# Performance work log

Hardware: AMD Instinct MI355X
Metric: run time of the kernel (lower is better)

Reference implementation:

```python
import jax, jax.numpy as jnp
import numpy as np

H, N_FULL, L_KERNEL, CHANNELS, RANK = 256, 128, 2048, 1, 1


def _legs_nplr(N, rank=1):
    # HiPPO-LegS transition + rank-1 correction -> NPLR (diag w - P P^*) form.
    q = np.arange(N, dtype=np.float64)
    col, row = np.meshgrid(q, q)
    r = 2 * q + 1
    M = -(np.where(row >= col, r, 0) - np.diag(q))
    T = np.sqrt(np.diag(2 * q + 1))
    A = T @ M @ np.linalg.inv(T)
    B = np.diag(T)                        # (N,)
    P = np.sqrt(0.5 + q)[None, :]         # (rank=1, N)
    AP = A + (P[:, :, None] * P[:, None, :]).sum(0)
    w, V = np.linalg.eig(AP)              # complex eigendecomposition
    w = w[0::2]                           # keep one of each conjugate pair -> N//2
    V = V[:, 0::2]
    V_inv = V.conj().T
    Bc = V_inv @ B.astype(V.dtype)        # (N//2,)
    Pc = (V_inv @ P.T.astype(V.dtype)).T  # (rank, N//2)
    return w, Pc, Bc


def _c2r(a):
    return jnp.stack([jnp.real(a), jnp.imag(a)], axis=-1).astype(jnp.float32)


def _r2c(a):
    return jax.lax.complex(a[..., 0], a[..., 1])


def setup_inputs() -> dict:
    key = jax.random.key(0)
    k1, k2 = jax.random.split(key)
    w, P, B = _legs_nplr(N_FULL, RANK)    # numpy complex128, half-size N = 64
    Nh = w.shape[-1]
    w = jnp.asarray(np.broadcast_to(w[None, :], (H, Nh)).copy())
    P = jnp.asarray(np.broadcast_to(P[:, None, :], (RANK, H, Nh)).copy())
    B = jnp.asarray(np.broadcast_to(B[None, None, :], (1, H, Nh)).copy())
    C = jax.random.normal(k1, (CHANNELS, H, Nh, 2), dtype=jnp.float32)
    log_dt = jax.random.uniform(k2, (H,), dtype=jnp.float32) * (
        float(np.log(0.1)) - float(np.log(0.001))) + float(np.log(0.001))
    return {
        'w_ri': _c2r(w), 'P_ri': _c2r(P), 'B_ri': _c2r(B),
        'C_ri': C, 'log_dt': log_dt, 'L': L_KERNEL,
    }


def reference(w_ri, P_ri, B_ri, C_ri, log_dt, L):
    w = _r2c(w_ri)        # (H, N) complex64
    P = _r2c(P_ri)        # (r, H, N)
    B = _r2c(B_ri)        # (1, H, N)
    C = _r2c(C_ri)        # (c, H, N)
    dt = jnp.exp(log_dt)  # (H,)
    Lh = L // 2 + 1
    # FFT nodes, processed through the bilinear transform
    omega = jnp.exp((-2j * np.pi / L) * jnp.arange(Lh, dtype=jnp.float32))
    z = 2 * (1 - omega) / (1 + omega)
    w_dt = w * dt[:, None]                               # incorporate dt into A
    Bcat = jnp.concatenate([B, P], axis=0)               # (1+r, H, N)
    Ccat = jnp.concatenate([C, jnp.conj(P)], axis=0)     # (c+r, H, N)  Q = conj(P)
    v = Bcat[:, None] * Ccat[None]                       # (1+r, c+r, H, N)
    # conjugate-symmetric extension to the full 2N poles
    v2 = jnp.concatenate([v, jnp.conj(v)], axis=-1)      # (1+r, c+r, H, 2N)
    w2 = jnp.concatenate([w_dt, jnp.conj(w_dt)], axis=-1)  # (H, 2N)
    # naive Cauchy sum (the O(N*L) hotspot): (1+r, c+r, H, Lh)
    r = (v2[..., None] / (z - w2[..., None])).sum(axis=-2)
    r = r * dt[None, None, :, None]
    # rank-1 Woodbury correction for the low-rank term
    k_f = r[:-1, :-1] - r[:-1, -1:] * r[-1:, :-1] / (1 + r[-1:, -1:])
    # final bilinear-transform correction, then frequency -> time
    k_f = k_f * 2 / (1 + omega)
    k = jnp.fft.irfft(k_f, n=L, axis=-1)                 # (1, c, H, L) real
    return k[0].astype(jnp.float32)                      # (c, H, L)
```

## Files before the change

kernel.cpp:

```cpp
#include <hip/hip_runtime.h>

#define NH 64
#define LFULL 2048
#define MH 1024
#define PI_F 3.14159265358979323846f
#define ANG_HALF 1.5339807878856412e-3f

typedef __attribute__((ext_vector_type(2))) float f32x2;
typedef __attribute__((ext_vector_type(4))) float f32x4;

#define SV(v, i, j) __builtin_shufflevector((v), (v), (i), (j))
#define PK_FMA(acc, a_, b_) asm("v_pk_fma_f32 %0, %1, %2, %0" : "+v"(acc) : "v"(a_), "v"(b_))

struct QS2 { f32x2 s1, s2, s3, s4; };

__global__ __launch_bounds__(512) void hippo_ssk(
    const float* __restrict__ w_ri,
    const float* __restrict__ P_ri,
    const float* __restrict__ B_ri,
    const float* __restrict__ C_ri,
    const float* __restrict__ log_dt,
    float* __restrict__ out)
{
    __shared__ __attribute__((aligned(16))) float pole2[NH][20];
    __shared__ float2 Kf[MH + 1];
    __shared__ float2 bufA[MH];
    __shared__ float2 bufB[MH];

    const int h   = blockIdx.x;
    const int tid = threadIdx.x;

    if (tid < NH) {
        const float dt = __expf(log_dt[h]);
        const float2 w = ((const float2*)w_ri)[h*NH + tid];
        const float2 P = ((const float2*)P_ri)[h*NH + tid];
        const float2 B = ((const float2*)B_ri)[h*NH + tid];
        const float2 C = ((const float2*)C_ri)[h*NH + tid];
        const float a = w.x * dt, b = w.y * dt;
        const float v00r = (B.x*C.x - B.y*C.y) * dt;
        const float v00i = (B.x*C.y + B.y*C.x) * dt;
        const float v01r = (B.x*P.x + B.y*P.y) * dt;
        const float v01i = (B.y*P.x - B.x*P.y) * dt;
        const float v10r = (P.x*C.x - P.y*C.y) * dt;
        const float v10i = (P.x*C.y + P.y*C.x) * dt;
        const float v11  = (P.x*P.x + P.y*P.y) * dt;
        float* pp = pole2[tid];
        const float na2 = -2.f*a;
        const float m2  = fmaf(a, a, b*b);
        const float p1_00 = -2.f*fmaf(v00r, a, v00i*b), p0_00 = 2.f*v00r;
        const float p1_01 = -2.f*fmaf(v01r, a, v01i*b), p0_01 = 2.f*v01r;
        const float p1_10 = -2.f*fmaf(v10r, a, v10i*b), p0_10 = 2.f*v10r;
        const float p1_11 = -2.f*v11*a,                 p0_11 = 2.f*v11;
        pp[0]=na2;   pp[1]=na2;   pp[2]=m2;    pp[3]=m2;
        pp[4]=p1_00; pp[5]=p1_00; pp[6]=p0_00; pp[7]=p0_00;
        pp[8]=p1_01; pp[9]=p1_01; pp[10]=p0_01; pp[11]=p0_01;
        pp[12]=p1_10; pp[13]=p1_10; pp[14]=p0_10; pp[15]=p0_10;
        pp[16]=p1_11; pp[17]=p1_11; pp[18]=p0_11; pp[19]=p0_11;
        float s = v00r;
        #pragma unroll
        for (int off = 32; off > 0; off >>= 1) s += __shfl_down(s, off, 64);
        if (tid == 0) Kf[MH] = make_float2(s, 0.f);
    }
    __syncthreads();

    {
        const int lA = tid;
        const int lB = tid + 512;
        float shA, chA, shB, chB;
        __sincosf(ANG_HALF * (float)lA, &shA, &chA);
        __sincosf(ANG_HALF * (float)lB, &shB, &chB);
        const float yA = 2.f * shA * __builtin_amdgcn_rcpf(chA);
        const float yB = 2.f * shB * __builtin_amdgcn_rcpf(chB);
        f32x2 yp;  yp.x = yA;        yp.y = yB;
        f32x2 ny2; ny2.x = -yA*yA;   ny2.y = -yB*yB;
        QS2 a00 = {{0,0},{0,0},{0,0},{0,0}};
        QS2 a01 = {{0,0},{0,0},{0,0},{0,0}};
        QS2 a10 = {{0,0},{0,0},{0,0},{0,0}};
        QS2 a11 = {{0,0},{0,0},{0,0},{0,0}};
        #pragma unroll 4
        for (int n = 0; n < NH; ++n) {
            const f32x4 c0 = *reinterpret_cast<const f32x4*>(&pole2[n][0]);
            const f32x4 c1 = *reinterpret_cast<const f32x4*>(&pole2[n][4]);
            const f32x4 c2 = *reinterpret_cast<const f32x4*>(&pole2[n][8]);
            const f32x4 c3 = *reinterpret_cast<const f32x4*>(&pole2[n][12]);
            const f32x4 c4 = *reinterpret_cast<const f32x4*>(&pole2[n][16]);
            const f32x2 dr = SV(c0, 2, 3) + ny2;
            const f32x2 di = SV(c0, 0, 1) * yp;
            const f32x2 den = dr*dr + di*di;
            f32x2 t;
            t.x = __builtin_amdgcn_rcpf(den.x);
            t.y = __builtin_amdgcn_rcpf(den.y);
            const f32x2 U = dr * t;
            const f32x2 V = di * t;
            PK_FMA(a00.s1, SV(c1,0,1), U);  PK_FMA(a00.s2, SV(c1,0,1), V);
            PK_FMA(a00.s3, SV(c1,2,3), U);  PK_FMA(a00.s4, SV(c1,2,3), V);
            PK_FMA(a01.s1, SV(c2,0,1), U);  PK_FMA(a01.s2, SV(c2,0,1), V);
            PK_FMA(a01.s3, SV(c2,2,3), U);  PK_FMA(a01.s4, SV(c2,2,3), V);
            PK_FMA(a10.s1, SV(c3,0,1), U);  PK_FMA(a10.s2, SV(c3,0,1), V);
            PK_FMA(a10.s3, SV(c3,2,3), U);  PK_FMA(a10.s4, SV(c3,2,3), V);
            PK_FMA(a11.s1, SV(c4,0,1), U);  PK_FMA(a11.s2, SV(c4,0,1), V);
            PK_FMA(a11.s3, SV(c4,2,3), U);  PK_FMA(a11.s4, SV(c4,2,3), V);
        }
        const f32x2 r00r = yp*a00.s4 + a00.s1;
        const f32x2 r00i = yp*a00.s3 - a00.s2;
        const f32x2 r01r = yp*a01.s4 + a01.s1;
        const f32x2 r01i = yp*a01.s3 - a01.s2;
        const f32x2 r10r = yp*a10.s4 + a10.s1;
        const f32x2 r10i = yp*a10.s3 - a10.s2;
        const f32x2 r11r = yp*a11.s4 + a11.s1;
        const f32x2 r11i = yp*a11.s3 - a11.s2;
        const f32x2 nr = r01r*r10r - r01i*r10i;
        const f32x2 ni = r01r*r10i + r01i*r10r;
        const f32x2 dw = 1.f + r11r;
        const f32x2 dv = r11i;
        f32x2 id2;
        id2.x = 1.f / (dw.x*dw.x + dv.x*dv.x);
        id2.y = 1.f / (dw.y*dw.y + dv.y*dv.y);
        const f32x2 cr = (nr*dw + ni*dv)*id2;
        const f32x2 ci = (ni*dw - nr*dv)*id2;
        const f32x2 k0r = r00r - cr;
        const f32x2 k0i = r00i - ci;
        const f32x2 hy = 0.5f*yp;
        Kf[lA] = make_float2(k0r.x - k0i.x*hy.x, k0i.x + k0r.x*hy.x);
        Kf[lB] = make_float2(k0r.y - k0i.y*hy.y, k0i.y + k0r.y*hy.y);
    }
    __syncthreads();

    #pragma unroll
    for (int i = 0; i < 2; ++i) {
        const int k = tid + 512*i;
        float2 Xk = Kf[k];
        if (k == 0) Xk.y = 0.f;
        float2 Xc = Kf[MH - k];
        Xc.y = -Xc.y;
        const float Er = 0.5f*(Xk.x + Xc.x), Ei = 0.5f*(Xk.y + Xc.y);
        const float Tr = 0.5f*(Xk.x - Xc.x), Ti = 0.5f*(Xk.y - Xc.y);
        const float ang = (PI_F/1024.f) * (float)k;
        float sa, ca;
        __sincosf(ang, &sa, &ca);
        const float Or = ca*Tr - sa*Ti;
        const float Oi = ca*Ti + sa*Tr;
        bufA[k] = make_float2(Er - Oi, Ei + Or);
    }
    __syncthreads();

    float2* Xb = bufA;
    float2* Yb = bufB;
    int m = 1;
    #pragma unroll
    for (int st = 0; st < 10; ++st) {
        const int jm = tid & ~(m - 1);
        const float ang = (PI_F/512.f) * (float)jm;
        float sw, cw;
        __sincosf(ang, &sw, &cw);
        const float2 c0 = Xb[tid];
        const float2 c1 = Xb[tid + 512];
        const int o0 = tid + jm;
        const float drr = c0.x - c1.x, dii = c0.y - c1.y;
        Yb[o0]     = make_float2(c0.x + c1.x, c0.y + c1.y);
        Yb[o0 + m] = make_float2(cw*drr - sw*dii, cw*dii + sw*drr);
        __syncthreads();
        float2* t = Xb; Xb = Yb; Yb = t;
        m <<= 1;
    }

    const float sc = 1.0f/1024.0f;
    float2* op2 = (float2*)(out + (size_t)h * LFULL);
    const float2 z0 = Xb[tid];
    op2[tid]       = make_float2(z0.x*sc, z0.y*sc);
    const float2 z1 = Xb[tid + 512];
    op2[tid + 512] = make_float2(z1.x*sc, z1.y*sc);
}

extern "C" void kernel_launch(void* const* d_in, const int* in_sizes, int n_in,
                              void* d_out, int out_size, void* d_ws, size_t ws_size,
                              hipStream_t stream) {
    const float* w_ri   = (const float*)d_in[0];
    const float* P_ri   = (const float*)d_in[1];
    const float* B_ri   = (const float*)d_in[2];
    const float* C_ri   = (const float*)d_in[3];
    const float* log_dt = (const float*)d_in[4];
    float* out = (float*)d_out;
    const int Hn = in_sizes[4];
    hippo_ssk<<<dim3(Hn), dim3(512), 0, stream>>>(w_ri, P_ri, B_ri, C_ri, log_dt, out);
}
```

Measured before the change: 17.04 us.

## Compact pole table, share reciprocal, fold FFT end stages, recurse twiddles

```diff
diff --git a/kernel.cpp b/kernel.cpp
--- a/kernel.cpp
+++ b/kernel.cpp
@@ -5,14 +5,18 @@
 #define MH 1024
 #define PI_F 3.14159265358979323846f
 #define ANG_HALF 1.5339807878856412e-3f
+#define ANG_3A   3.0679615757712823e-3f
 
 typedef __attribute__((ext_vector_type(2))) float f32x2;
 typedef __attribute__((ext_vector_type(4))) float f32x4;
 
-#define SV(v, i, j) __builtin_shufflevector((v), (v), (i), (j))
-#define PK_FMA(acc, a_, b_) asm("v_pk_fma_f32 %0, %1, %2, %0" : "+v"(acc) : "v"(a_), "v"(b_))
-
-struct QS2 { f32x2 s1, s2, s3, s4; };
+#define SV2(v, i, j) __builtin_shufflevector((v), (v), (i), (j))
+#define PK_FMA_LO(acc, pair, uv) \
+    asm("v_pk_fma_f32 %0, %1, %2, %0 op_sel:[0,0,0] op_sel_hi:[0,1,1]" \
+        : "+v"(acc) : "v"(pair), "v"(uv))
+#define PK_FMA_HI(acc, pair, uv) \
+    asm("v_pk_fma_f32 %0, %1, %2, %0 op_sel:[1,0,0] op_sel_hi:[1,1,1]" \
+        : "+v"(acc) : "v"(pair), "v"(uv))
 
 __global__ __launch_bounds__(512) void hippo_ssk(
     const float* __restrict__ w_ri,
@@ -22,20 +26,21 @@
     const float* __restrict__ log_dt,
     float* __restrict__ out)
 {
-    __shared__ __attribute__((aligned(16))) float pole2[NH][20];
+    __shared__ __attribute__((aligned(16))) float pole2[NH][12];
     __shared__ float2 Kf[MH + 1];
     __shared__ float2 bufA[MH];
     __shared__ float2 bufB[MH];
 
-    const int h   = blockIdx.x;
-    const int tid = threadIdx.x;
-
-    if (tid < NH) {
+    const int h    = blockIdx.x;
+    const int tid  = threadIdx.x;
+    const int lane = tid & 63;
+
+    {
         const float dt = __expf(log_dt[h]);
-        const float2 w = ((const float2*)w_ri)[h*NH + tid];
-        const float2 P = ((const float2*)P_ri)[h*NH + tid];
-        const float2 B = ((const float2*)B_ri)[h*NH + tid];
-        const float2 C = ((const float2*)C_ri)[h*NH + tid];
+        const float2 w = ((const float2*)w_ri)[h*NH + lane];
+        const float2 P = ((const float2*)P_ri)[h*NH + lane];
+        const float2 B = ((const float2*)B_ri)[h*NH + lane];
+        const float2 C = ((const float2*)C_ri)[h*NH + lane];
         const float a = w.x * dt, b = w.y * dt;
         const float v00r = (B.x*C.x - B.y*C.y) * dt;
         const float v00i = (B.x*C.y + B.y*C.x) * dt;
@@ -44,24 +49,17 @@
         const float v10r = (P.x*C.x - P.y*C.y) * dt;
         const float v10i = (P.x*C.y + P.y*C.x) * dt;
         const float v11  = (P.x*P.x + P.y*P.y) * dt;
-        float* pp = pole2[tid];
-        const float na2 = -2.f*a;
-        const float m2  = fmaf(a, a, b*b);
-        const float p1_00 = -2.f*fmaf(v00r, a, v00i*b), p0_00 = 2.f*v00r;
-        const float p1_01 = -2.f*fmaf(v01r, a, v01i*b), p0_01 = 2.f*v01r;
-        const float p1_10 = -2.f*fmaf(v10r, a, v10i*b), p0_10 = 2.f*v10r;
-        const float p1_11 = -2.f*v11*a,                 p0_11 = 2.f*v11;
-        pp[0]=na2;   pp[1]=na2;   pp[2]=m2;    pp[3]=m2;
-        pp[4]=p1_00; pp[5]=p1_00; pp[6]=p0_00; pp[7]=p0_00;
-        pp[8]=p1_01; pp[9]=p1_01; pp[10]=p0_01; pp[11]=p0_01;
-        pp[12]=p1_10; pp[13]=p1_10; pp[14]=p0_10; pp[15]=p0_10;
-        pp[16]=p1_11; pp[17]=p1_11; pp[18]=p0_11; pp[19]=p0_11;
+        float4* pp = (float4*)pole2[lane];
+        pp[0] = make_float4(-2.f*a, fmaf(a, a, b*b),
+                            -2.f*fmaf(v00r, a, v00i*b), 2.f*v00r);
+        pp[1] = make_float4(-2.f*fmaf(v01r, a, v01i*b), 2.f*v01r,
+                            -2.f*fmaf(v10r, a, v10i*b), 2.f*v10r);
+        *(float2*)&pole2[lane][8] = make_float2(-2.f*v11*a, 2.f*v11);
         float s = v00r;
         #pragma unroll
         for (int off = 32; off > 0; off >>= 1) s += __shfl_down(s, off, 64);
         if (tid == 0) Kf[MH] = make_float2(s, 0.f);
     }
-    __syncthreads();
 
     {
         const int lA = tid;
@@ -71,51 +69,57 @@
         __sincosf(ANG_HALF * (float)lB, &shB, &chB);
         const float yA = 2.f * shA * __builtin_amdgcn_rcpf(chA);
         const float yB = 2.f * shB * __builtin_amdgcn_rcpf(chB);
-        f32x2 yp;  yp.x = yA;        yp.y = yB;
-        f32x2 ny2; ny2.x = -yA*yA;   ny2.y = -yB*yB;
-        QS2 a00 = {{0,0},{0,0},{0,0},{0,0}};
-        QS2 a01 = {{0,0},{0,0},{0,0},{0,0}};
-        QS2 a10 = {{0,0},{0,0},{0,0},{0,0}};
-        QS2 a11 = {{0,0},{0,0},{0,0},{0,0}};
+        f32x2 yp;  yp.x = yA;       yp.y = yB;
+        f32x2 ny2; ny2.x = -yA*yA;  ny2.y = -yB*yB;
+        f32x2 s1_00={0,0}, s2_00={0,0}, s3_00={0,0}, s4_00={0,0};
+        f32x2 s1_01={0,0}, s2_01={0,0}, s3_01={0,0}, s4_01={0,0};
+        f32x2 s1_10={0,0}, s2_10={0,0}, s3_10={0,0}, s4_10={0,0};
+        f32x2 s1_11={0,0}, s2_11={0,0}, s3_11={0,0}, s4_11={0,0};
         #pragma unroll 4
         for (int n = 0; n < NH; ++n) {
-            const f32x4 c0 = *reinterpret_cast<const f32x4*>(&pole2[n][0]);
-            const f32x4 c1 = *reinterpret_cast<const f32x4*>(&pole2[n][4]);
-            const f32x4 c2 = *reinterpret_cast<const f32x4*>(&pole2[n][8]);
-            const f32x4 c3 = *reinterpret_cast<const f32x4*>(&pole2[n][12]);
-            const f32x4 c4 = *reinterpret_cast<const f32x4*>(&pole2[n][16]);
-            const f32x2 dr = SV(c0, 2, 3) + ny2;
-            const f32x2 di = SV(c0, 0, 1) * yp;
+            const f32x4 q0 = *reinterpret_cast<const f32x4*>(&pole2[n][0]);
+            const f32x4 q1 = *reinterpret_cast<const f32x4*>(&pole2[n][4]);
+            const f32x2 q2 = *reinterpret_cast<const f32x2*>(&pole2[n][8]);
+            const f32x2 nm  = SV2(q0, 0, 1);
+            const f32x2 p00 = SV2(q0, 2, 3);
+            const f32x2 p01 = SV2(q1, 0, 1);
+            const f32x2 p10 = SV2(q1, 2, 3);
+            f32x2 dr, di;
+            asm("v_pk_add_f32 %0, %1, %2 op_sel:[1,0] op_sel_hi:[1,1]"
+                : "=v"(dr) : "v"(nm), "v"(ny2));
+            asm("v_pk_mul_f32 %0, %1, %2 op_sel:[0,0] op_sel_hi:[0,1]"
+                : "=v"(di) : "v"(nm), "v"(yp));
             const f32x2 den = dr*dr + di*di;
-            f32x2 t;
-            t.x = __builtin_amdgcn_rcpf(den.x);
-            t.y = __builtin_amdgcn_rcpf(den.y);
+            const float pp  = den.x * den.y;
+            const float ipp = __builtin_amdgcn_rcpf(pp);
+            f32x2 t;  t.x = ipp * den.y;  t.y = ipp * den.x;
             const f32x2 U = dr * t;
             const f32x2 V = di * t;
-            PK_FMA(a00.s1, SV(c1,0,1), U);  PK_FMA(a00.s2, SV(c1,0,1), V);
-            PK_FMA(a00.s3, SV(c1,2,3), U);  PK_FMA(a00.s4, SV(c1,2,3), V);
-            PK_FMA(a01.s1, SV(c2,0,1), U);  PK_FMA(a01.s2, SV(c2,0,1), V);
-            PK_FMA(a01.s3, SV(c2,2,3), U);  PK_FMA(a01.s4, SV(c2,2,3), V);
-            PK_FMA(a10.s1, SV(c3,0,1), U);  PK_FMA(a10.s2, SV(c3,0,1), V);
-            PK_FMA(a10.s3, SV(c3,2,3), U);  PK_FMA(a10.s4, SV(c3,2,3), V);
-            PK_FMA(a11.s1, SV(c4,0,1), U);  PK_FMA(a11.s2, SV(c4,0,1), V);
-            PK_FMA(a11.s3, SV(c4,2,3), U);  PK_FMA(a11.s4, SV(c4,2,3), V);
+            PK_FMA_LO(s1_00, p00, U);  PK_FMA_LO(s2_00, p00, V);
+            PK_FMA_HI(s3_00, p00, U);  PK_FMA_HI(s4_00, p00, V);
+            PK_FMA_LO(s1_01, p01, U);  PK_FMA_LO(s2_01, p01, V);
+            PK_FMA_HI(s3_01, p01, U);  PK_FMA_HI(s4_01, p01, V);
+            PK_FMA_LO(s1_10, p10, U);  PK_FMA_LO(s2_10, p10, V);
+            PK_FMA_HI(s3_10, p10, U);  PK_FMA_HI(s4_10, p10, V);
+            PK_FMA_LO(s1_11, q2,  U);  PK_FMA_LO(s2_11, q2,  V);
+            PK_FMA_HI(s3_11, q2,  U);  PK_FMA_HI(s4_11, q2,  V);
         }
-        const f32x2 r00r = yp*a00.s4 + a00.s1;
-        const f32x2 r00i = yp*a00.s3 - a00.s2;
-        const f32x2 r01r = yp*a01.s4 + a01.s1;
-        const f32x2 r01i = yp*a01.s3 - a01.s2;
-        const f32x2 r10r = yp*a10.s4 + a10.s1;
-        const f32x2 r10i = yp*a10.s3 - a10.s2;
-        const f32x2 r11r = yp*a11.s4 + a11.s1;
-        const f32x2 r11i = yp*a11.s3 - a11.s2;
+        const f32x2 r00r = yp*s4_00 + s1_00;
+        const f32x2 r00i = yp*s3_00 - s2_00;
+        const f32x2 r01r = yp*s4_01 + s1_01;
+        const f32x2 r01i = yp*s3_01 - s2_01;
+        const f32x2 r10r = yp*s4_10 + s1_10;
+        const f32x2 r10i = yp*s3_10 - s2_10;
+        const f32x2 r11r = yp*s4_11 + s1_11;
+        const f32x2 r11i = yp*s3_11 - s2_11;
         const f32x2 nr = r01r*r10r - r01i*r10i;
         const f32x2 ni = r01r*r10i + r01i*r10r;
         const f32x2 dw = 1.f + r11r;
         const f32x2 dv = r11i;
+        const f32x2 d2 = dw*dw + dv*dv;
         f32x2 id2;
-        id2.x = 1.f / (dw.x*dw.x + dv.x*dv.x);
-        id2.y = 1.f / (dw.y*dw.y + dv.y*dv.y);
+        id2.x = __builtin_amdgcn_rcpf(d2.x);
+        id2.y = __builtin_amdgcn_rcpf(d2.y);
         const f32x2 cr = (nr*dw + ni*dv)*id2;
         const f32x2 ci = (ni*dw - nr*dv)*id2;
         const f32x2 k0r = r00r - cr;
@@ -126,50 +130,70 @@
     }
     __syncthreads();
 
-    #pragma unroll
-    for (int i = 0; i < 2; ++i) {
-        const int k = tid + 512*i;
-        float2 Xk = Kf[k];
-        if (k == 0) Xk.y = 0.f;
-        float2 Xc = Kf[MH - k];
-        Xc.y = -Xc.y;
-        const float Er = 0.5f*(Xk.x + Xc.x), Ei = 0.5f*(Xk.y + Xc.y);
-        const float Tr = 0.5f*(Xk.x - Xc.x), Ti = 0.5f*(Xk.y - Xc.y);
-        const float ang = (PI_F/1024.f) * (float)k;
+    float2 wtw;
+    {
         float sa, ca;
-        __sincosf(ang, &sa, &ca);
-        const float Or = ca*Tr - sa*Ti;
-        const float Oi = ca*Ti + sa*Tr;
-        bufA[k] = make_float2(Er - Oi, Ei + Or);
+        __sincosf(ANG_3A * (float)tid, &sa, &ca);
+        float2 Xk = Kf[tid];
+        if (tid == 0) Xk.y = 0.f;
+        float2 Xc = Kf[MH - tid];  Xc.y = -Xc.y;
+        const float Er0 = 0.5f*(Xk.x + Xc.x), Ei0 = 0.5f*(Xk.y + Xc.y);
+        const float Tr0 = 0.5f*(Xk.x - Xc.x), Ti0 = 0.5f*(Xk.y - Xc.y);
+        const float Or0 = ca*Tr0 - sa*Ti0;
+        const float Oi0 = ca*Ti0 + sa*Tr0;
+        const float2 Z0 = make_float2(Er0 - Oi0, Ei0 + Or0);
+        const float2 Xk1 = Kf[tid + 512];
+        float2 Xc1 = Kf[512 - tid];  Xc1.y = -Xc1.y;
+        const float Er1 = 0.5f*(Xk1.x + Xc1.x), Ei1 = 0.5f*(Xk1.y + Xc1.y);
+        const float Tr1 = 0.5f*(Xk1.x - Xc1.x), Ti1 = 0.5f*(Xk1.y - Xc1.y);
+        const float Or1 = -sa*Tr1 - ca*Ti1;
+        const float Oi1 = -sa*Ti1 + ca*Tr1;
+        const float2 Z1 = make_float2(Er1 - Oi1, Ei1 + Or1);
+        const float cw = ca*ca - sa*sa;
+        const float sw = 2.f*ca*sa;
+        bufA[2*tid]     = make_float2(Z0.x + Z1.x, Z0.y + Z1.y);
+        const float drr = Z0.x - Z1.x, dii = Z0.y - Z1.y;
+        bufA[2*tid + 1] = make_float2(cw*drr - sw*dii, cw*dii + sw*drr);
+        wtw = make_float2(cw, sw);
+        const float mc = (tid & 1) ? 0.99998118f : 1.f;
+        const float ms = (tid & 1) ? 0.00613588f : 0.f;
+        wtw = make_float2(wtw.x*mc + wtw.y*ms, wtw.y*mc - wtw.x*ms);
     }
     __syncthreads();
 
-    float2* Xb = bufA;
-    float2* Yb = bufB;
-    int m = 1;
-    #pragma unroll
-    for (int st = 0; st < 10; ++st) {
-        const int jm = tid & ~(m - 1);
-        const float ang = (PI_F/512.f) * (float)jm;
-        float sw, cw;
-        __sincosf(ang, &sw, &cw);
+    {
+        const float CM_C[7] = {0.99992470f, 0.99969882f, 0.99879546f, 0.99518473f,
+                               0.98078528f, 0.92387953f, 0.70710678f};
+        const float CM_S[7] = {0.01227154f, 0.02454123f, 0.04906767f, 0.09801714f,
+                               0.19509032f, 0.38268343f, 0.70710678f};
+        float2* Xb = bufA;
+        float2* Yb = bufB;
+        int m = 2;
+        #pragma unroll
+        for (int st = 0; st < 8; ++st) {
+            const int jm = tid & ~(m - 1);
+            const float2 c0 = Xb[tid];
+            const float2 c1 = Xb[tid + 512];
+            const int o0 = tid + jm;
+            const float drr = c0.x - c1.x, dii = c0.y - c1.y;
+            Yb[o0]     = make_float2(c0.x + c1.x, c0.y + c1.y);
+            Yb[o0 + m] = make_float2(wtw.x*drr - wtw.y*dii, wtw.x*dii + wtw.y*drr);
+            if (st < 7) {
+                const float mc = (tid & m) ? CM_C[st] : 1.f;
+                const float ms = (tid & m) ? CM_S[st] : 0.f;
+                wtw = make_float2(wtw.x*mc + wtw.y*ms, wtw.y*mc - wtw.x*ms);
+            }
+            __syncthreads();
+            float2* t = Xb; Xb = Yb; Yb = t;
+            m <<= 1;
+        }
+        const float sc = 1.0f/1024.0f;
+        float2* op2 = (float2*)(out + (size_t)h * LFULL);
         const float2 c0 = Xb[tid];
         const float2 c1 = Xb[tid + 512];
-        const int o0 = tid + jm;
-        const float drr = c0.x - c1.x, dii = c0.y - c1.y;
-        Yb[o0]     = make_float2(c0.x + c1.x, c0.y + c1.y);
-        Yb[o0 + m] = make_float2(cw*drr - sw*dii, cw*dii + sw*drr);
-        __syncthreads();
-        float2* t = Xb; Xb = Yb; Yb = t;
-        m <<= 1;
-    }
-
-    const float sc = 1.0f/1024.0f;
-    float2* op2 = (float2*)(out + (size_t)h * LFULL);
-    const float2 z0 = Xb[tid];
-    op2[tid]       = make_float2(z0.x*sc, z0.y*sc);
-    const float2 z1 = Xb[tid + 512];
-    op2[tid + 512] = make_float2(z1.x*sc, z1.y*sc);
+        op2[tid]       = make_float2((c0.x + c1.x)*sc, (c0.y + c1.y)*sc);
+        op2[tid + 512] = make_float2((c0.x - c1.x)*sc, (c0.y - c1.y)*sc);
+    }
 }
 
 extern "C" void kernel_launch(void* const* d_in, const int* in_sizes, int n_in,
```

Result: no change. 17.19 us (+0.9%).
